# Performance work log

Hardware: AMD Instinct MI355X
Metric: run time of the kernel (lower is better)

Reference implementation:

```python
import jax, jax.numpy as jnp
import numpy as np

H = 4            # attention heads
C = 128          # hidden_size (per-head channels; concat=False -> mean over heads)
ET = 5           # edge types
IN = 512         # input feature dim
NCLS = 153
N_TOTAL = 100000
N_SRC = (40000, 20000)
N_DST = (30000, 10000)
BATCH = (25000, 8000)
E = (200000, 80000)
EPS = 1e-5


def bn(x, g, b):
    # BatchNorm1d, training-mode batch statistics (biased var), affine
    mu = x.mean(0)
    var = x.var(0)
    return (x - mu) / jnp.sqrt(var + EPS) * g + b


def gat(x_src, src, dst, n_dst, W, att_s, att_d, bias):
    # PyG GATConv, bipartite (x_src, x_src[:n_dst]), shared lin, concat=False
    x = (x_src @ W).reshape(-1, H, C)            # [Ns, H, C]
    a_s = (x * att_s).sum(-1)                    # [Ns, H]
    a_d = (x[:n_dst] * att_d).sum(-1)            # [Nd, H]
    logits = jax.nn.leaky_relu(a_s[src] + a_d[dst], 0.2)   # [E, H]
    m = jax.ops.segment_max(logits, dst, num_segments=n_dst)
    e = jnp.exp(logits - m[dst])
    s = jax.ops.segment_sum(e, dst, num_segments=n_dst)
    coef = e / jnp.maximum(s[dst], 1e-16)        # segment softmax over in-edges
    out = jax.ops.segment_sum(coef[:, :, None] * x[src], dst, num_segments=n_dst)
    return out.mean(1) + bias                    # [Nd, C]


def _layer(feature, li, nodes_idx, src, dst, Ws, bs, bng, bnb, Wg, attS, attD, bg, wp, bp, pg, pb):
    batch, n_dst = BATCH[li], N_DST[li]
    skip = jax.nn.elu(bn(feature @ Ws + bs, bng[0], bnb[0]))
    feats = [skip[:batch]]
    for e2 in range(ET):  # small fixed set of structurally distinct edge types
        xs = feature[nodes_idx[e2]]
        o = gat(xs, src[e2], dst[e2], n_dst, Wg[e2], attS[e2], attD[e2], bg[e2])
        feats.append(jax.nn.elu(bn(o, bng[e2 + 1], bnb[e2 + 1]))[:batch])
    temp = jnp.stack(feats, 1)                   # [batch, ET+1, C]
    attn = jax.nn.softmax(temp @ wp + bp, axis=1)  # [batch, ET+1, 1]
    sk = jnp.einsum('bp,bpc->bc', attn[..., 0], temp)
    return bn(sk, pg, pb)                        # dropout is identity at inference


def setup_inputs():
    key = jax.random.key(0)
    keys = iter(jax.random.split(key, 48))
    def nrm(shape, scale):
        return jax.random.normal(next(keys), shape, dtype=jnp.float32) * scale
    def ri(shape, hi):
        return jax.random.randint(next(keys), shape, 0, hi, dtype=jnp.int32)
    inp = {}
    inp['feature'] = nrm((N_TOTAL, IN), 1.0)
    inp['nodes_idx0'] = ri((ET, N_SRC[0]), N_TOTAL)
    inp['edge_src0'] = ri((ET, E[0]), N_SRC[0])
    inp['edge_dst0'] = jnp.sort(ri((ET, E[0]), N_DST[0]), axis=-1)
    inp['nodes_idx1'] = ri((ET, N_SRC[1]), BATCH[0])
    inp['edge_src1'] = ri((ET, E[1]), N_SRC[1])
    inp['edge_dst1'] = jnp.sort(ri((ET, E[1]), N_DST[1]), axis=-1)
    for l, din in ((0, IN), (1, C)):
        s = str(l)
        sc = 1.0 / float(np.sqrt(din))
        inp['W_skip' + s] = nrm((din, C), sc)
        inp['b_skip' + s] = jnp.zeros((C,), jnp.float32)
        inp['bn_g' + s] = jnp.ones((ET + 1, C), jnp.float32)
        inp['bn_b' + s] = jnp.zeros((ET + 1, C), jnp.float32)
        inp['Wg' + s] = nrm((ET, din, H * C), sc)
        inp['attS' + s] = nrm((ET, H, C), 0.1)
        inp['attD' + s] = nrm((ET, H, C), 0.1)
        inp['bg' + s] = jnp.zeros((ET, C), jnp.float32)
        inp['wp' + s] = nrm((C, 1), 1.0 / float(np.sqrt(C)))
        inp['bp' + s] = jnp.zeros((1,), jnp.float32)
        inp['pg' + s] = jnp.ones((C,), jnp.float32)
        inp['pb' + s] = jnp.zeros((C,), jnp.float32)
    inp['Wm1'] = nrm((C, C), 1.0 / float(np.sqrt(C)))
    inp['bm1'] = jnp.zeros((C,), jnp.float32)
    inp['mg'] = jnp.ones((C,), jnp.float32)
    inp['mb'] = jnp.zeros((C,), jnp.float32)
    inp['Wm2'] = nrm((C, NCLS), 1.0 / float(np.sqrt(C)))
    inp['bm2'] = jnp.zeros((NCLS,), jnp.float32)
    return inp


def reference(feature, nodes_idx0, edge_src0, edge_dst0, nodes_idx1, edge_src1, edge_dst1,
              W_skip0, b_skip0, bn_g0, bn_b0, Wg0, attS0, attD0, bg0, wp0, bp0, pg0, pb0,
              W_skip1, b_skip1, bn_g1, bn_b1, Wg1, attS1, attD1, bg1, wp1, bp1, pg1, pb1,
              Wm1, bm1, mg, mb, Wm2, bm2):
    f = _layer(feature, 0, nodes_idx0, edge_src0, edge_dst0,
               W_skip0, b_skip0, bn_g0, bn_b0, Wg0, attS0, attD0, bg0, wp0, bp0, pg0, pb0)
    f = _layer(f, 1, nodes_idx1, edge_src1, edge_dst1,
               W_skip1, b_skip1, bn_g1, bn_b1, Wg1, attS1, attD1, bg1, wp1, bp1, pg1, pb1)
    h = jax.nn.relu(bn(f @ Wm1 + bm1, mg, mb))
    return h @ Wm2 + bm2
```

## Files before the change

kernel.cpp:

```cpp
#include <hip/hip_runtime.h>
#include <math.h>

#define EPSV 1e-5f
#define NSTATB 960

typedef __attribute__((ext_vector_type(8))) short short8;
typedef __attribute__((ext_vector_type(4))) float floatx4;
typedef _Float16 half2v __attribute__((ext_vector_type(2)));

__device__ __forceinline__ float waveSum(float v) {
#pragma unroll
  for (int off = 32; off > 0; off >>= 1) v += __shfl_xor(v, off, 64);
  return v;
}

__device__ __forceinline__ unsigned bfr(float f) {
  union { float f; unsigned u; } v;
  v.f = f;
  return (v.u + 0x7FFFu + ((v.u >> 16) & 1u)) >> 16;
}

__device__ __forceinline__ void gload16(const short* g, short* l) {
  __builtin_amdgcn_global_load_lds(
      (const __attribute__((address_space(1))) void*)g,
      (__attribute__((address_space(3))) void*)l, 16, 0, 0);
}

__global__ __launch_bounds__(256) void conv_bf16(const float* __restrict__ x,
                                                 short* __restrict__ y, long n4) {
  long i = (long)blockIdx.x * 256 + threadIdx.x;
  long stride = (long)gridDim.x * 256;
  for (; i < n4; i += stride) {
    float4 v = reinterpret_cast<const float4*>(x)[i];
    short4 o;
    o.x = (short)bfr(v.x);
    o.y = (short)bfr(v.y);
    o.z = (short)bfr(v.z);
    o.w = (short)bfr(v.w);
    reinterpret_cast<short4*>(y)[i] = o;
  }
}

__global__ __launch_bounds__(256) void wT_bf16(const float* __restrict__ W0,
                                               short* __restrict__ Wt0, int K, int N,
                                               long wz) {
  const float* W = W0 + (size_t)blockIdx.z * wz;
  short* Wt = Wt0 + (size_t)blockIdx.z * wz;
  __shared__ short t[32][33];
  int k0 = blockIdx.x * 32, n0 = blockIdx.y * 32;
  int x = threadIdx.x & 31, y = threadIdx.x >> 5;
#pragma unroll
  for (int dy = 0; dy < 32; dy += 8) {
    int k = k0 + y + dy, n = n0 + x;
    t[y + dy][x] = (k < K && n < N) ? (short)bfr(W[(size_t)k * N + n]) : (short)0;
  }
  __syncthreads();
#pragma unroll
  for (int dy = 0; dy < 32; dy += 8) {
    int n = n0 + y + dy, k = k0 + x;
    if (n < N && k < K) Wt[(size_t)n * K + k] = t[x][y + dy];
  }
}

__global__ __launch_bounds__(512) void gemm_mfma(
    const short* __restrict__ A, const short* __restrict__ Wt0,
    const float* __restrict__ bias, float* __restrict__ Y0,
    _Float16* __restrict__ Yh0, const int* __restrict__ idx0,
    int M, int K, int N, int mTiles, int nTiles,
    long wtZ, long yZ, int idxZ,
    const float* __restrict__ attS0, const float* __restrict__ attD0,
    float* __restrict__ a_s0, float* __restrict__ a_d0, int n_dst) {
  __shared__ short Alds[3][128 * 32];
  __shared__ short Blds[3][128 * 32];
  __shared__ float sred[128][4];
  int z = blockIdx.z;
  int mt, nt;
  if (nTiles == 1) {
    mt = blockIdx.x;
    nt = 0;
  } else {
    int id = blockIdx.x;
    int slot = id >> 3;
    nt = slot & 3;
    mt = ((slot >> 2) << 3) + (id & 7);
  }
  if (mt >= mTiles) return;
  const short* Wt = Wt0 + (size_t)z * wtZ;
  const int* idx = idx0 ? (idx0 + (size_t)z * idxZ) : nullptr;
  int tid = threadIdx.x;
  int m0 = mt * 128, n0 = nt * 128;

  int srow = tid >> 2, sc = tid & 3;
  int swzc = sc ^ ((srow >> 1) & 3);
  int grow = m0 + srow;
  int ar = (grow < M) ? (idx ? idx[grow] : grow) : 0;
  const short* aSrc = A + (size_t)ar * K + swzc * 8;
  const short* bSrc = Wt + (size_t)(n0 + srow) * K + swzc * 8;
  int wv = tid >> 6, lane = tid & 63;
  int dOff = wv * 512;

  int wm = (wv & 1) * 64, wn = (wv >> 1) * 32;
  int lr = lane & 15, quad = lane >> 4;
  int aoff[4], boff[2];
#pragma unroll
  for (int i = 0; i < 4; i++) {
    int R = wm + i * 16 + lr;
    aoff[i] = R * 32 + ((quad ^ ((R >> 1) & 3)) << 3);
  }
#pragma unroll
  for (int j = 0; j < 2; j++) {
    int R = wn + j * 16 + lr;
    boff[j] = R * 32 + ((quad ^ ((R >> 1) & 3)) << 3);
  }

  floatx4 acc[4][2];
#pragma unroll
  for (int i = 0; i < 4; i++)
#pragma unroll
    for (int j = 0; j < 2; j++) acc[i][j] = (floatx4)0.f;

  auto stage = [&](int slot, int k) {
    gload16(aSrc + k, &Alds[slot][dOff]);
    gload16(bSrc + k, &Blds[slot][dOff]);
  };
  auto compute = [&](int slot) {
    const short* Ab = Alds[slot];
    const short* Bb = Blds[slot];
    short8 af[4], bfv[2];
#pragma unroll
    for (int i = 0; i < 4; i++)
      af[i] = *reinterpret_cast<const short8*>(&Ab[aoff[i]]);
#pragma unroll
    for (int j = 0; j < 2; j++)
      bfv[j] = *reinterpret_cast<const short8*>(&Bb[boff[j]]);
#pragma unroll
    for (int i = 0; i < 4; i++)
#pragma unroll
      for (int j = 0; j < 2; j++)
        acc[i][j] = __builtin_amdgcn_mfma_f32_16x16x32_bf16(af[i], bfv[j],
                                                            acc[i][j], 0, 0, 0);
  };

  stage(0, 0);
  stage(1, 32);
  int NT = K >> 5;
  int cur = 0, nxt = 2;
  for (int t = 0; t < NT; ++t) {
    if (t + 1 < NT) {
      asm volatile("s_waitcnt vmcnt(2)" : : : "memory");
    } else {
      asm volatile("s_waitcnt vmcnt(0)" : : : "memory");
    }
    __builtin_amdgcn_s_barrier();
    __builtin_amdgcn_sched_barrier(0);
    if (t + 2 < NT) stage(nxt, 32 * (t + 2));
    compute(cur);
    cur = (cur == 2) ? 0 : cur + 1;
    nxt = (nxt == 2) ? 0 : nxt + 1;
  }

#pragma unroll
  for (int i = 0; i < 4; i++) {
#pragma unroll
    for (int j = 0; j < 2; j++) {
      int n = n0 + wn + j * 16 + lr;
      float bv = bias ? bias[n] : 0.f;
#pragma unroll
      for (int r = 0; r < 4; r++) {
        int m = m0 + wm + i * 16 + quad * 4 + r;
        if (m < M) {
          float v = acc[i][j][r] + bv;
          if (Yh0) {
            _Float16* Yh = Yh0 + (size_t)z * yZ;
            Yh[(size_t)m * N + n] = (_Float16)v;
          } else {
            float* Y = Y0 + (size_t)z * yZ;
            Y[(size_t)m * N + n] = v;
          }
        }
      }
    }
  }
  if (attS0) {
    int h = nt;
    const float* aSb = attS0 + z * 512 + h * 128;
    const float* aDb = attD0 + z * 512 + h * 128;
    float* asv = a_s0 + (size_t)z * M * 4;
    float* adv = a_d0 + (size_t)z * n_dst * 4;
#pragma unroll
    for (int p = 0; p < 2; p++) {
      const float* av = p ? aDb : aSb;
      float w0a = av[wn + lr], w1a = av[wn + 16 + lr];
#pragma unroll
      for (int i = 0; i < 4; i++) {
#pragma unroll
        for (int r = 0; r < 4; r++) {
          float v = acc[i][0][r] * w0a + acc[i][1][r] * w1a;
          v += __shfl_xor(v, 1, 64);
          v += __shfl_xor(v, 2, 64);
          v += __shfl_xor(v, 4, 64);
          v += __shfl_xor(v, 8, 64);
          if (lr == 0) sred[wm + i * 16 + quad * 4 + r][wv >> 1] = v;
        }
      }
      __syncthreads();
      if (tid < 128) {
        int m = m0 + tid;
        if (m < M) {
          float s = sred[tid][0] + sred[tid][1] + sred[tid][2] + sred[tid][3];
          if (p == 0) asv[(size_t)m * 4 + h] = s;
          else if (m < n_dst) adv[(size_t)m * 4 + h] = s;
        }
      }
      __syncthreads();
    }
  }
}

__global__ __launch_bounds__(256) void gemm_bias(
    const float* __restrict__ A, const float* __restrict__ W,
    const float* __restrict__ bias, float* __restrict__ Y,
    const int* __restrict__ idx, int M, int K, int N) {
  __shared__ float As[16][65];
  __shared__ float Bs[16][64];
  int tid = threadIdx.x;
  int tx = tid & 15, ty = tid >> 4;
  int m0 = blockIdx.x * 64, n0 = blockIdx.y * 64;
  float acc[4][4] = {};
  for (int k0 = 0; k0 < K; k0 += 16) {
    for (int l = tid; l < 64 * 16; l += 256) {
      int r = l >> 4, kk = l & 15;
      int row = m0 + r;
      float v = 0.f;
      if (row < M) {
        int ar = idx ? idx[row] : row;
        v = A[(size_t)ar * K + k0 + kk];
      }
      As[kk][r] = v;
    }
    for (int l = tid; l < 16 * 64; l += 256) {
      int kk = l >> 6, n = l & 63;
      int col = n0 + n;
      Bs[kk][n] = (col < N) ? W[(size_t)(k0 + kk) * N + col] : 0.f;
    }
    __syncthreads();
#pragma unroll
    for (int kk = 0; kk < 16; kk++) {
      float a[4], b[4];
#pragma unroll
      for (int i = 0; i < 4; i++) a[i] = As[kk][ty + 16 * i];
#pragma unroll
      for (int j = 0; j < 4; j++) b[j] = Bs[kk][tx + 16 * j];
#pragma unroll
      for (int i = 0; i < 4; i++)
#pragma unroll
        for (int j = 0; j < 4; j++) acc[i][j] += a[i] * b[j];
    }
    __syncthreads();
  }
#pragma unroll
  for (int i = 0; i < 4; i++) {
    int m = m0 + ty + 16 * i;
    if (m >= M) continue;
#pragma unroll
    for (int j = 0; j < 4; j++) {
      int n = n0 + tx + 16 * j;
      if (n < N) Y[(size_t)m * N + n] = acc[i][j] + (bias ? bias[n] : 0.f);
    }
  }
}

__global__ void build_starts(const int* __restrict__ dst0, int E, int n_dst,
                             int* __restrict__ starts0) {
  const int* dst = dst0 + (size_t)blockIdx.y * E;
  int* starts = starts0 + (size_t)blockIdx.y * (n_dst + 1);
  int k = blockIdx.x * 256 + threadIdx.x;
  if (k > E) return;
  if (k == 0) {
    int d0 = dst[0];
    for (int j = 0; j <= d0; j++) starts[j] = 0;
  } else if (k < E) {
    int d = dst[k], dp = dst[k - 1];
    for (int j = dp + 1; j <= d; j++) starts[j] = k;
  } else {
    int dl = dst[E - 1];
    for (int j = dl + 1; j <= n_dst; j++) starts[j] = E;
  }
}

__global__ void edge_logits(const int* __restrict__ src0, const int* __restrict__ dst0,
                            const float* __restrict__ a_s0, const float* __restrict__ a_d0,
                            float* __restrict__ logits0, int E, int asZ, int adZ) {
  int z = blockIdx.y;
  const int* src = src0 + (size_t)z * E;
  const int* dst = dst0 + (size_t)z * E;
  const float* a_s = a_s0 + (size_t)z * asZ;
  const float* a_d = a_d0 + (size_t)z * adZ;
  float* logits = logits0 + (size_t)z * E * 4;
  int k = blockIdx.x * 256 + threadIdx.x;
  if (k >= E) return;
  int s = src[k], d = dst[k];
#pragma unroll
  for (int h = 0; h < 4; h++) {
    float v = a_s[s * 4 + h] + a_d[d * 4 + h];
    v = (v >= 0.f) ? v : 0.2f * v;
    logits[k * 4 + h] = v;
  }
}

__global__ void node_ms(const float* __restrict__ logits0, const int* __restrict__ starts0,
                        float* __restrict__ ms0, int n_dst, int E) {
  int z = blockIdx.y;
  const float* logits = logits0 + (size_t)z * E * 4;
  const int* starts = starts0 + (size_t)z * (n_dst + 1);
  float* ms = ms0 + (size_t)z * n_dst * 8;
  int t = blockIdx.x * 256 + threadIdx.x;
  int j = t >> 2, h = t & 3;
  if (j >= n_dst) return;
  int r0 = starts[j], r1 = starts[j + 1];
  float m = -1e30f;
  for (int k = r0; k < r1; k++) m = fmaxf(m, logits[k * 4 + h]);
  float s = 0.f;
  for (int k = r0; k < r1; k++) s += __expf(logits[k * 4 + h] - m);
  ms[j * 8 + h] = m;
  ms[j * 8 + 4 + h] = s;
}

__global__ __launch_bounds__(64) void gat_aggregate(
    const _Float16* __restrict__ x0, const float* __restrict__ lg0,
    const int* __restrict__ src0, const int* __restrict__ starts0,
    const float* __restrict__ ms0, const float* __restrict__ bg0,
    float* __restrict__ o0, int n_dst, long xZ, int E) {
  int z = blockIdx.y;
  const _Float16* x = x0 + (size_t)z * xZ;
  const float* lg = lg0 + (size_t)z * E * 4;
  const int* src = src0 + (size_t)z * E;
  const int* starts = starts0 + (size_t)z * (n_dst + 1);
  const float* ms = ms0 + (size_t)z * n_dst * 8;
  const float* bg = bg0 + z * 128;
  float* o = o0 + (size_t)z * (size_t)n_dst * 128;
  int j = blockIdx.x;
  int t = threadIdx.x;
  int r0 = starts[j], r1 = starts[j + 1];
  float m0 = ms[j * 8 + 0], m1 = ms[j * 8 + 1];
  float m2 = ms[j * 8 + 2], m3 = ms[j * 8 + 3];
  float i0 = 1.f / fmaxf(ms[j * 8 + 4], 1e-16f);
  float i1 = 1.f / fmaxf(ms[j * 8 + 5], 1e-16f);
  float i2 = 1.f / fmaxf(ms[j * 8 + 6], 1e-16f);
  float i3 = 1.f / fmaxf(ms[j * 8 + 7], 1e-16f);
  float a00 = 0.f, a01 = 0.f, a10 = 0.f, a11 = 0.f;
  float a20 = 0.f, a21 = 0.f, a30 = 0.f, a31 = 0.f;
  for (int k = r0; k < r1; k++) {
    int s = src[k];
    const half2v* xr = reinterpret_cast<const half2v*>(x + (size_t)s * 512);
    half2v v0 = xr[t];
    half2v v1 = xr[64 + t];
    half2v v2 = xr[128 + t];
    half2v v3 = xr[192 + t];
    float c0 = __expf(lg[k * 4 + 0] - m0) * i0;
    float c1 = __expf(lg[k * 4 + 1] - m1) * i1;
    float c2 = __expf(lg[k * 4 + 2] - m2) * i2;
    float c3 = __expf(lg[k * 4 + 3] - m3) * i3;
    a00 += c0 * (float)v0[0];
    a01 += c0 * (float)v0[1];
    a10 += c1 * (float)v1[0];
    a11 += c1 * (float)v1[1];
    a20 += c2 * (float)v2[0];
    a21 += c2 * (float)v2[1];
    a30 += c3 * (float)v3[0];
    a31 += c3 * (float)v3[1];
  }
  float2 out;
  out.x = 0.25f * (a00 + a10 + a20 + a30) + bg[2 * t];
  out.y = 0.25f * (a01 + a11 + a21 + a31) + bg[2 * t + 1];
  *reinterpret_cast<float2*>(&o[(size_t)j * 128 + 2 * t]) = out;
}

__global__ __launch_bounds__(128) void bn_partial(const float* __restrict__ x0, long xZ,
                                                  float* __restrict__ partial0, int N) {
  const float* x = x0 + (size_t)blockIdx.y * xZ;
  float* partial = partial0 + (size_t)blockIdx.y * (NSTATB * 256);
  int c = threadIdx.x;
  float s = 0.f, ss = 0.f;
  for (int r = blockIdx.x; r < N; r += gridDim.x) {
    float v = x[(size_t)r * 128 + c];
    s += v;
    ss += v * v;
  }
  partial[blockIdx.x * 256 + c] = s;
  partial[blockIdx.x * 256 + 128 + c] = ss;
}

__global__ __launch_bounds__(64) void bn_finalize(const float* __restrict__ partial0,
                                                  int G, int N, float* __restrict__ stats0) {
  const float* partial = partial0 + (size_t)blockIdx.y * (NSTATB * 256);
  float* stats = stats0 + blockIdx.y * 256;
  int c = blockIdx.x;
  int lane = threadIdx.x;
  float s = 0.f, ss = 0.f;
  for (int b = lane; b < G; b += 64) {
    s += partial[b * 256 + c];
    ss += partial[b * 256 + 128 + c];
  }
  s = waveSum(s);
  ss = waveSum(ss);
  if (lane == 0) {
    float mu = s / (float)N;
    float var = ss / (float)N - mu * mu;
    stats[c] = mu;
    stats[128 + c] = rsqrtf(var + EPSV);
  }
}

__global__ __launch_bounds__(128) void bn_apply(
    const float* __restrict__ x0, long xZ, const float* __restrict__ stats0,
    const float* __restrict__ g0, const float* __restrict__ b0, int gz,
    float* __restrict__ y0, short* __restrict__ yb0, long yZ, int M,
    int ostride, int act) {
  int z = blockIdx.y;
  const float* x = x0 + (size_t)z * xZ;
  const float* stats = stats0 + z * 256;
  const float* g = g0 + z * gz;
  const float* b = b0 + z * gz;
  int r = blockIdx.x;
  int c = threadIdx.x;
  if (r >= M) return;
  float v = x[(size_t)r * 128 + c];
  v = (v - stats[c]) * stats[128 + c] * g[c] + b[c];
  if (act == 1) v = (v > 0.f) ? v : (__expf(v) - 1.f);
  if (act == 2) v = fmaxf(v, 0.f);
  if (yb0) {
    short* yb = yb0 + (size_t)z * yZ;
    yb[(size_t)r * ostride + c] = (short)bfr(v);
  } else {
    float* y = y0 + (size_t)z * yZ;
    y[(size_t)r * ostride + c] = v;
  }
}

__global__ __launch_bounds__(128) void pool_attn(
    const float* __restrict__ temp, const float* __restrict__ wp,
    const float* __restrict__ bp, float* __restrict__ sk, int batch) {
  int b = blockIdx.x, c = threadIdx.x;
  int lane = c & 63, wid = c >> 6;
  __shared__ float red[12];
  const float* tr = temp + (size_t)b * 768;
  float wpc = wp[c];
  float t[6];
#pragma unroll
  for (int p = 0; p < 6; p++) t[p] = tr[p * 128 + c];
#pragma unroll
  for (int p = 0; p < 6; p++) {
    float v = waveSum(t[p] * wpc);
    if (lane == 0) red[wid * 6 + p] = v;
  }
  __syncthreads();
  float z[6], m = -1e30f;
#pragma unroll
  for (int p = 0; p < 6; p++) {
    z[p] = red[p] + red[6 + p] + bp[0];
    m = fmaxf(m, z[p]);
  }
  float es = 0.f;
#pragma unroll
  for (int p = 0; p < 6; p++) {
    z[p] = __expf(z[p] - m);
    es += z[p];
  }
  float inv = 1.f / es;
  float o = 0.f;
#pragma unroll
  for (int p = 0; p < 6; p++) o += z[p] * inv * t[p];
  sk[(size_t)b * 128 + c] = o;
}

extern "C" void kernel_launch(void* const* d_in, const int* in_sizes, int n_in,
                              void* d_out, int out_size, void* d_ws, size_t ws_size,
                              hipStream_t stream) {
  const float* feature = (const float*)d_in[0];
  const int* nodes_idx[2] = {(const int*)d_in[1], (const int*)d_in[4]};
  const int* edge_src[2] = {(const int*)d_in[2], (const int*)d_in[5]};
  const int* edge_dst[2] = {(const int*)d_in[3], (const int*)d_in[6]};
  const float *Wsk[2], *bsk[2], *bng[2], *bnb[2], *Wg[2], *attS[2], *attD[2],
      *bg[2], *wp[2], *bp[2], *pg[2], *pb[2];
  for (int l = 0; l < 2; l++) {
    int base = 7 + l * 12;
    Wsk[l] = (const float*)d_in[base + 0];
    bsk[l] = (const float*)d_in[base + 1];
    bng[l] = (const float*)d_in[base + 2];
    bnb[l] = (const float*)d_in[base + 3];
    Wg[l] = (const float*)d_in[base + 4];
    attS[l] = (const float*)d_in[base + 5];
    attD[l] = (const float*)d_in[base + 6];
    bg[l] = (const float*)d_in[base + 7];
    wp[l] = (const float*)d_in[base + 8];
    bp[l] = (const float*)d_in[base + 9];
    pg[l] = (const float*)d_in[base + 10];
    pb[l] = (const float*)d_in[base + 11];
  }
  const float* Wm1 = (const float*)d_in[31];
  const float* bm1 = (const float*)d_in[32];
  const float* mg = (const float*)d_in[33];
  const float* mb = (const float*)d_in[34];
  const float* Wm2 = (const float*)d_in[35];
  const float* bm2 = (const float*)d_in[36];

  float* ws = (float*)d_ws;
  float* bufG5 = ws;   ws += 102400000;
  float* bufSkip = ws; ws += 12800000;
  float* bufO5 = ws;   ws += 19200000;
  float* temp = ws;    ws += 19200000;
  float* f1 = ws;      ws += 1024000;
  float* bufH = ws;    ws += 1024000;
  float* a_s5 = ws;    ws += 800000;
  float* a_d5 = ws;    ws += 600000;
  float* logi5 = ws;   ws += 4000000;
  float* ms5 = ws;     ws += 1200000;
  float* part = ws;    ws += 5 * NSTATB * 256;
  float* stats = ws;   ws += 5 * 256;
  int* starts5 = (int*)ws; ws += 150080;
  short* featB = (short*)ws; ws += 25600000;
  short* f0b = (short*)ws;   ws += 1600000;
  short* wt_sk0 = (short*)ws; ws += 32768;
  short* wt_g0 = (short*)ws;  ws += 655360;
  short* wt_sk1 = (short*)ws; ws += 8192;
  short* wt_g1 = (short*)ws;  ws += 163840;
  _Float16* bufG5h = (_Float16*)bufG5;

  auto cdiv = [](int a, int b) { return (a + b - 1) / b; };

  conv_bf16<<<2048, 256, 0, stream>>>(feature, featB, 100000L * 512 / 4);
  wT_bf16<<<dim3(16, 4, 1), 256, 0, stream>>>(Wsk[0], wt_sk0, 512, 128, 0);
  wT_bf16<<<dim3(16, 16, 5), 256, 0, stream>>>(Wg[0], wt_g0, 512, 512, 512L * 512);
  wT_bf16<<<dim3(4, 4, 1), 256, 0, stream>>>(Wsk[1], wt_sk1, 128, 128, 0);
  wT_bf16<<<dim3(4, 16, 5), 256, 0, stream>>>(Wg[1], wt_g1, 128, 512, 512L * 128);

  auto run_layer = [&](const short* Xb, int Nf, int din, int li, float* fout,
                       short* foutb, const short* wt_sk, const short* wt_g) {
    const int Nsrc = (li == 0) ? 40000 : 20000;
    const int n_dst = (li == 0) ? 30000 : 10000;
    const int batch = (li == 0) ? 25000 : 8000;
    const int E = (li == 0) ? 200000 : 80000;
    const int mtS = cdiv(Nf, 128);
    const int mtG = cdiv(Nsrc, 128);
    const int GpG = cdiv(mtG, 8) * 8;

    gemm_mfma<<<dim3(mtS, 1, 1), 512, 0, stream>>>(
        Xb, wt_sk, bsk[li], bufSkip, nullptr, nullptr, Nf, din, 128, mtS, 1,
        0, 0, 0, nullptr, nullptr, nullptr, nullptr, 0);
    bn_partial<<<dim3(NSTATB, 1), 128, 0, stream>>>(bufSkip, 0, part, Nf);
    bn_finalize<<<dim3(128, 1), 64, 0, stream>>>(part, NSTATB, Nf, stats);
    bn_apply<<<dim3(batch, 1), 128, 0, stream>>>(bufSkip, 0, stats, bng[li],
                                                 bnb[li], 0, temp, nullptr, 0,
                                                 batch, 768, 1);

    gemm_mfma<<<dim3(GpG * 4, 1, 5), 512, 0, stream>>>(
        Xb, wt_g, nullptr, nullptr, bufG5h, nodes_idx[li], Nsrc, din, 512,
        mtG, 4, (long)din * 512, (long)Nsrc * 512, Nsrc,
        attS[li], attD[li], a_s5, a_d5, n_dst);
    build_starts<<<dim3(cdiv(E + 1, 256), 5), 256, 0, stream>>>(edge_dst[li], E,
                                                                n_dst, starts5);
    edge_logits<<<dim3(cdiv(E, 256), 5), 256, 0, stream>>>(
        edge_src[li], edge_dst[li], a_s5, a_d5, logi5, E, Nsrc * 4, n_dst * 4);
    node_ms<<<dim3(cdiv(n_dst * 4, 256), 5), 256, 0, stream>>>(logi5, starts5,
                                                               ms5, n_dst, E);
    gat_aggregate<<<dim3(n_dst, 5), 64, 0, stream>>>(
        bufG5h, logi5, edge_src[li], starts5, ms5, bg[li], bufO5, n_dst,
        (long)Nsrc * 512, E);
    bn_partial<<<dim3(NSTATB, 5), 128, 0, stream>>>(bufO5, (long)n_dst * 128,
                                                    part, n_dst);
    bn_finalize<<<dim3(128, 5), 64, 0, stream>>>(part, NSTATB, n_dst, stats);
    bn_apply<<<dim3(batch, 5), 128, 0, stream>>>(
        bufO5, (long)n_dst * 128, stats, bng[li] + 128, bnb[li] + 128, 128,
        temp + 128, nullptr, 128, batch, 768, 1);

    pool_attn<<<batch, 128, 0, stream>>>(temp, wp[li], bp[li], bufSkip, batch);
    bn_partial<<<dim3(NSTATB, 1), 128, 0, stream>>>(bufSkip, 0, part, batch);
    bn_finalize<<<dim3(128, 1), 64, 0, stream>>>(part, NSTATB, batch, stats);
    bn_apply<<<dim3(batch, 1), 128, 0, stream>>>(bufSkip, 0, stats, pg[li], pb[li],
                                                 0, fout, foutb, 0, batch, 128, 0);
  };

  run_layer(featB, 100000, 512, 0, nullptr, f0b, wt_sk0, wt_g0);
  run_layer(f0b, 25000, 128, 1, f1, nullptr, wt_sk1, wt_g1);

  gemm_bias<<<dim3(cdiv(8000, 64), 2), 256, 0, stream>>>(f1, Wm1, bm1, bufSkip,
                                                         nullptr, 8000, 128, 128);
  bn_partial<<<dim3(NSTATB, 1), 128, 0, stream>>>(bufSkip, 0, part, 8000);
  bn_finalize<<<dim3(128, 1), 64, 0, stream>>>(part, NSTATB, 8000, stats);
  bn_apply<<<8000, 128, 0, stream>>>(bufSkip, 0, stats, mg, mb, 0, bufH,
                                     nullptr, 0, 8000, 128, 2);
  gemm_bias<<<dim3(cdiv(8000, 64), 3), 256, 0, stream>>>(
      bufH, Wm2, bm2, (float*)d_out, nullptr, 8000, 128, 153);
}
```

Measured before the change: 1.301 ms.

## Enlarge MFMA GEMM block tile to 256 rows and hoist CSR start building

Result: no change. 1.311 ms (+0.8%).

```diff
diff --git a/kernel.cpp b/kernel.cpp
--- a/kernel.cpp
+++ b/kernel.cpp
@@ -62,7 +62,9 @@
   }
 }
 
-__global__ __launch_bounds__(512) void gemm_mfma(
+#define ASZ (256 * 32)
+#define BSZ (128 * 32)
+__global__ __launch_bounds__(512, 4) void gemm_mfma(
     const short* __restrict__ A, const short* __restrict__ Wt0,
     const float* __restrict__ bias, float* __restrict__ Y0,
     _Float16* __restrict__ Yh0, const int* __restrict__ idx0,
@@ -70,9 +72,9 @@
     long wtZ, long yZ, int idxZ,
     const float* __restrict__ attS0, const float* __restrict__ attD0,
     float* __restrict__ a_s0, float* __restrict__ a_d0, int n_dst) {
-  __shared__ short Alds[3][128 * 32];
-  __shared__ short Blds[3][128 * 32];
-  __shared__ float sred[128][4];
+  __shared__ short Alds[3 * ASZ];
+  __shared__ short Blds[3 * BSZ];
+  __shared__ float sred[256][2];
   int z = blockIdx.z;
   int mt, nt;
   if (nTiles == 1) {
@@ -88,55 +90,63 @@
   const short* Wt = Wt0 + (size_t)z * wtZ;
   const int* idx = idx0 ? (idx0 + (size_t)z * idxZ) : nullptr;
   int tid = threadIdx.x;
-  int m0 = mt * 128, n0 = nt * 128;
+  int m0 = mt * 256, n0 = nt * 128;
 
   int srow = tid >> 2, sc = tid & 3;
-  int swzc = sc ^ ((srow >> 1) & 3);
-  int grow = m0 + srow;
-  int ar = (grow < M) ? (idx ? idx[grow] : grow) : 0;
-  const short* aSrc = A + (size_t)ar * K + swzc * 8;
-  const short* bSrc = Wt + (size_t)(n0 + srow) * K + swzc * 8;
+  int rA0 = srow, rA1 = 128 + srow;
+  int swzA0 = sc ^ ((rA0 >> 1) & 3);
+  int swzA1 = sc ^ ((rA1 >> 1) & 3);
+  int swzB = swzA0;
+  int gr0 = m0 + rA0, gr1 = m0 + rA1;
+  int ar0 = (gr0 < M) ? (idx ? idx[gr0] : gr0) : 0;
+  int ar1 = (gr1 < M) ? (idx ? idx[gr1] : gr1) : 0;
+  const short* aSrc0 = A + (size_t)ar0 * K + swzA0 * 8;
+  const short* aSrc1 = A + (size_t)ar1 * K + swzA1 * 8;
+  const short* bSrc = Wt + (size_t)(n0 + srow) * K + swzB * 8;
   int wv = tid >> 6, lane = tid & 63;
-  int dOff = wv * 512;
-
-  int wm = (wv & 1) * 64, wn = (wv >> 1) * 32;
+  int dA0 = wv * 512;
+  int dA1 = 4096 + wv * 512;
+  int dB = wv * 512;
+
+  int wm = (wv & 3) * 64, wn = (wv >> 2) * 64;
   int lr = lane & 15, quad = lane >> 4;
-  int aoff[4], boff[2];
+  int aoff[4], boff[4];
 #pragma unroll
   for (int i = 0; i < 4; i++) {
     int R = wm + i * 16 + lr;
     aoff[i] = R * 32 + ((quad ^ ((R >> 1) & 3)) << 3);
   }
 #pragma unroll
-  for (int j = 0; j < 2; j++) {
+  for (int j = 0; j < 4; j++) {
     int R = wn + j * 16 + lr;
     boff[j] = R * 32 + ((quad ^ ((R >> 1) & 3)) << 3);
   }
 
-  floatx4 acc[4][2];
+  floatx4 acc[4][4];
 #pragma unroll
   for (int i = 0; i < 4; i++)
 #pragma unroll
-    for (int j = 0; j < 2; j++) acc[i][j] = (floatx4)0.f;
+    for (int j = 0; j < 4; j++) acc[i][j] = (floatx4)0.f;
 
   auto stage = [&](int slot, int k) {
-    gload16(aSrc + k, &Alds[slot][dOff]);
-    gload16(bSrc + k, &Blds[slot][dOff]);
+    gload16(aSrc0 + k, &Alds[slot * ASZ + dA0]);
+    gload16(aSrc1 + k, &Alds[slot * ASZ + dA1]);
+    gload16(bSrc + k, &Blds[slot * BSZ + dB]);
   };
   auto compute = [&](int slot) {
-    const short* Ab = Alds[slot];
-    const short* Bb = Blds[slot];
-    short8 af[4], bfv[2];
+    const short* Ab = &Alds[slot * ASZ];
+    const short* Bb = &Blds[slot * BSZ];
+    short8 af[4], bfv[4];
 #pragma unroll
     for (int i = 0; i < 4; i++)
       af[i] = *reinterpret_cast<const short8*>(&Ab[aoff[i]]);
 #pragma unroll
-    for (int j = 0; j < 2; j++)
+    for (int j = 0; j < 4; j++)
       bfv[j] = *reinterpret_cast<const short8*>(&Bb[boff[j]]);
 #pragma unroll
     for (int i = 0; i < 4; i++)
 #pragma unroll
-      for (int j = 0; j < 2; j++)
+      for (int j = 0; j < 4; j++)
         acc[i][j] = __builtin_amdgcn_mfma_f32_16x16x32_bf16(af[i], bfv[j],
                                                             acc[i][j], 0, 0, 0);
   };
@@ -147,7 +157,7 @@
   int cur = 0, nxt = 2;
   for (int t = 0; t < NT; ++t) {
     if (t + 1 < NT) {
-      asm volatile("s_waitcnt vmcnt(2)" : : : "memory");
+      asm volatile("s_waitcnt vmcnt(3)" : : : "memory");
     } else {
       asm volatile("s_waitcnt vmcnt(0)" : : : "memory");
     }
@@ -162,7 +172,7 @@
 #pragma unroll
   for (int i = 0; i < 4; i++) {
 #pragma unroll
-    for (int j = 0; j < 2; j++) {
+    for (int j = 0; j < 4; j++) {
       int n = n0 + wn + j * 16 + lr;
       float bv = bias ? bias[n] : 0.f;
 #pragma unroll
@@ -190,24 +200,27 @@
 #pragma unroll
     for (int p = 0; p < 2; p++) {
       const float* av = p ? aDb : aSb;
-      float w0a = av[wn + lr], w1a = av[wn + 16 + lr];
+      float w[4];
+#pragma unroll
+      for (int j = 0; j < 4; j++) w[j] = av[wn + j * 16 + lr];
 #pragma unroll
       for (int i = 0; i < 4; i++) {
 #pragma unroll
         for (int r = 0; r < 4; r++) {
-          float v = acc[i][0][r] * w0a + acc[i][1][r] * w1a;
+          float v = acc[i][0][r] * w[0] + acc[i][1][r] * w[1] +
+                    acc[i][2][r] * w[2] + acc[i][3][r] * w[3];
           v += __shfl_xor(v, 1, 64);
           v += __shfl_xor(v, 2, 64);
           v += __shfl_xor(v, 4, 64);
           v += __shfl_xor(v, 8, 64);
-          if (lr == 0) sred[wm + i * 16 + quad * 4 + r][wv >> 1] = v;
+          if (lr == 0) sred[wm + i * 16 + quad * 4 + r][wv >> 2] = v;
         }
       }
       __syncthreads();
-      if (tid < 128) {
+      if (tid < 256) {
         int m = m0 + tid;
         if (m < M) {
-          float s = sred[tid][0] + sred[tid][1] + sred[tid][2] + sred[tid][3];
+          float s = sred[tid][0] + sred[tid][1];
           if (p == 0) asv[(size_t)m * 4 + h] = s;
           else if (m < n_dst) adv[(size_t)m * 4 + h] = s;
         }
@@ -518,7 +531,8 @@
   float* ms5 = ws;     ws += 1200000;
   float* part = ws;    ws += 5 * NSTATB * 256;
   float* stats = ws;   ws += 5 * 256;
-  int* starts5 = (int*)ws; ws += 150080;
+  int* starts5a = (int*)ws; ws += 150080;
+  int* starts5b = (int*)ws; ws += 50080;
   short* featB = (short*)ws; ws += 25600000;
   short* f0b = (short*)ws;   ws += 1600000;
   short* wt_sk0 = (short*)ws; ws += 32768;
@@ -529,6 +543,10 @@
 
   auto cdiv = [](int a, int b) { return (a + b - 1) / b; };
 
+  build_starts<<<dim3(cdiv(200001, 256), 5), 256, 0, stream>>>(edge_dst[0],
+                                                               200000, 30000, starts5a);
+  build_starts<<<dim3(cdiv(80001, 256), 5), 256, 0, stream>>>(edge_dst[1],
+                                                              80000, 10000, starts5b);
   conv_bf16<<<2048, 256, 0, stream>>>(feature, featB, 100000L * 512 / 4);
   wT_bf16<<<dim3(16, 4, 1), 256, 0, stream>>>(Wsk[0], wt_sk0, 512, 128, 0);
   wT_bf16<<<dim3(16, 16, 5), 256, 0, stream>>>(Wg[0], wt_g0, 512, 512, 512L * 512);
@@ -536,13 +554,14 @@
   wT_bf16<<<dim3(4, 16, 5), 256, 0, stream>>>(Wg[1], wt_g1, 128, 512, 512L * 128);
 
   auto run_layer = [&](const short* Xb, int Nf, int din, int li, float* fout,
-                       short* foutb, const short* wt_sk, const short* wt_g) {
+                       short* foutb, const short* wt_sk, const short* wt_g,
+                       int* starts5) {
     const int Nsrc = (li == 0) ? 40000 : 20000;
     const int n_dst = (li == 0) ? 30000 : 10000;
     const int batch = (li == 0) ? 25000 : 8000;
     const int E = (li == 0) ? 200000 : 80000;
-    const int mtS = cdiv(Nf, 128);
-    const int mtG = cdiv(Nsrc, 128);
+    const int mtS = cdiv(Nf, 256);
+    const int mtG = cdiv(Nsrc, 256);
     const int GpG = cdiv(mtG, 8) * 8;
 
     gemm_mfma<<<dim3(mtS, 1, 1), 512, 0, stream>>>(
@@ -558,8 +577,6 @@
         Xb, wt_g, nullptr, nullptr, bufG5h, nodes_idx[li], Nsrc, din, 512,
         mtG, 4, (long)din * 512, (long)Nsrc * 512, Nsrc,
         attS[li], attD[li], a_s5, a_d5, n_dst);
-    build_starts<<<dim3(cdiv(E + 1, 256), 5), 256, 0, stream>>>(edge_dst[li], E,
-                                                                n_dst, starts5);
     edge_logits<<<dim3(cdiv(E, 256), 5), 256, 0, stream>>>(
         edge_src[li], edge_dst[li], a_s5, a_d5, logi5, E, Nsrc * 4, n_dst * 4);
     node_ms<<<dim3(cdiv(n_dst * 4, 256), 5), 256, 0, stream>>>(logi5, starts5,
@@ -581,8 +598,8 @@
                                                  0, fout, foutb, 0, batch, 128, 0);
   };
 
-  run_layer(featB, 100000, 512, 0, nullptr, f0b, wt_sk0, wt_g0);
-  run_layer(f0b, 25000, 128, 1, f1, nullptr, wt_sk1, wt_g1);
+  run_layer(featB, 100000, 512, 0, nullptr, f0b, wt_sk0, wt_g0, starts5a);
+  run_layer(f0b, 25000, 128, 1, f1, nullptr, wt_sk1, wt_g1, starts5b);
 
   gemm_bias<<<dim3(cdiv(8000, 64), 2), 256, 0, stream>>>(f1, Wm1, bm1, bufSkip,
                                                          nullptr, 8000, 128, 128);
```
